# Performance work log

Measured on AMD Instinct MI355X. Metric: run time of the kernel, lower is better.

## Reference

```python
import jax, jax.numpy as jnp
import numpy as np

D_MODEL = 256
D_FFN = 1024
N_HEADS = 8
N_LEVELS = 4
N_POINTS = 4
SPATIAL = np.array([[60, 100], [30, 50], [15, 25], [8, 13]], dtype=np.int32)  # (H, W) per level


def _layer_norm(x, g, b, eps=1e-5):
    mu = jnp.mean(x, axis=-1, keepdims=True)
    var = jnp.mean(jnp.square(x - mu), axis=-1, keepdims=True)
    return (x - mu) * jax.lax.rsqrt(var + eps) * g + b


def _bilinear_sample(v_l, loc, aw, H, W):
    # v_l: (B,H,W,h,hd); loc: (B,Lq,h,p,2) normalized [0,1]; aw: (B,Lq,h,p)
    B = v_l.shape[0]
    h = v_l.shape[3]
    x = loc[..., 0] * W - 0.5  # grid_sample align_corners=False convention
    y = loc[..., 1] * H - 0.5
    x0 = jnp.floor(x)
    y0 = jnp.floor(y)
    lx = x - x0
    ly = y - y0
    x0i = x0.astype(jnp.int32)
    y0i = y0.astype(jnp.int32)
    bi = jnp.arange(B)[:, None, None, None]
    hi = jnp.arange(h)[None, None, :, None]

    def g(xi, yi):
        valid = (xi >= 0) & (xi < W) & (yi >= 0) & (yi < H)
        xc = jnp.clip(xi, 0, W - 1)
        yc = jnp.clip(yi, 0, H - 1)
        return v_l[bi, yc, xc, hi] * valid[..., None].astype(v_l.dtype)  # zero padding

    w00 = (1 - lx) * (1 - ly)
    w01 = lx * (1 - ly)
    w10 = (1 - lx) * ly
    w11 = lx * ly
    samp = (g(x0i, y0i) * w00[..., None] + g(x0i + 1, y0i) * w01[..., None]
            + g(x0i, y0i + 1) * w10[..., None] + g(x0i + 1, y0i + 1) * w11[..., None])
    # weighted sum over sampling points -> (B,Lq,h,hd)
    return jnp.einsum('blhpd,blhp->blhd', samp, aw)


def _msda(q, val, ref, W_value, b_value, W_off, b_off, W_attn, b_attn, W_out, b_out):
    # mmcv MultiScaleDeformableAttention (batch_first, identity=query, eval-mode dropout)
    B, Lq, C = q.shape
    hd = C // N_HEADS
    v = (val @ W_value + b_value).reshape(B, -1, N_HEADS, hd)
    off = (q @ W_off + b_off).reshape(B, Lq, N_HEADS, N_LEVELS, N_POINTS, 2)
    aw = jax.nn.softmax((q @ W_attn + b_attn).reshape(B, Lq, N_HEADS, N_LEVELS * N_POINTS), axis=-1)
    aw = aw.reshape(B, Lq, N_HEADS, N_LEVELS, N_POINTS)
    normalizer = jnp.asarray(SPATIAL[:, ::-1].copy(), dtype=q.dtype)  # (levels, 2) = (W, H)
    loc = ref[:, :, None, :, None, :] + off / normalizer[None, None, None, :, None, :]
    out = jnp.zeros((B, Lq, N_HEADS, hd), q.dtype)
    start = 0
    for lvl in range(N_LEVELS):
        H, W = int(SPATIAL[lvl, 0]), int(SPATIAL[lvl, 1])
        v_l = v[:, start:start + H * W].reshape(B, H, W, N_HEADS, hd)
        start += H * W
        out = out + _bilinear_sample(v_l, loc[:, :, :, lvl], aw[:, :, :, lvl], H, W)
    return q + out.reshape(B, Lq, C) @ W_out + b_out  # identity + output_proj


def setup_inputs() -> dict:
    key = jax.random.key(0)
    ks = jax.random.split(key, 16)
    bs, cams, nq = 1, 6, 6400
    l = int(SPATIAL.prod(axis=1).sum())
    s = 0.02
    inp = {
        'query': jax.random.normal(ks[0], (bs, nq, D_MODEL), jnp.float32),
        'key': jax.random.normal(ks[1], (bs, cams, l, D_MODEL), jnp.float32),
        'value': jax.random.normal(ks[2], (bs, cams, l, D_MODEL), jnp.float32),
        'reference_points_cam': jax.random.uniform(ks[3], (cams, bs, nq, N_LEVELS, 2), jnp.float32),
        'spatial_shapes': jnp.asarray(SPATIAL),
        'level_start_index': jnp.asarray(np.concatenate([[0], np.cumsum(SPATIAL.prod(axis=1))[:-1]]).astype(np.int32)),
        'bev_mask': jax.random.randint(ks[4], (cams, bs, nq, 4), 0, 2).astype(jnp.int32),
        'W_value': jax.random.normal(ks[5], (D_MODEL, D_MODEL), jnp.float32) * s,
        'b_value': jnp.zeros((D_MODEL,), jnp.float32),
        'W_off': jax.random.normal(ks[6], (D_MODEL, N_HEADS * N_LEVELS * N_POINTS * 2), jnp.float32) * s,
        'b_off': jax.random.normal(ks[7], (N_HEADS * N_LEVELS * N_POINTS * 2,), jnp.float32) * s,
        'W_attn': jax.random.normal(ks[8], (D_MODEL, N_HEADS * N_LEVELS * N_POINTS), jnp.float32) * s,
        'b_attn': jnp.zeros((N_HEADS * N_LEVELS * N_POINTS,), jnp.float32),
        'W_out': jax.random.normal(ks[9], (D_MODEL, D_MODEL), jnp.float32) * s,
        'b_out': jnp.zeros((D_MODEL,), jnp.float32),
        'ln1_g': jnp.ones((D_MODEL,), jnp.float32),
        'ln1_b': jnp.zeros((D_MODEL,), jnp.float32),
        'W1': jax.random.normal(ks[10], (D_MODEL, D_FFN), jnp.float32) * s,
        'b1': jnp.zeros((D_FFN,), jnp.float32),
        'W2': jax.random.normal(ks[11], (D_FFN, D_MODEL), jnp.float32) * s,
        'b2': jnp.zeros((D_MODEL,), jnp.float32),
        'ln2_g': jnp.ones((D_MODEL,), jnp.float32),
        'ln2_b': jnp.zeros((D_MODEL,), jnp.float32),
    }
    return inp


def reference(query, key, value, reference_points_cam, spatial_shapes, level_start_index, bev_mask,
              W_value, b_value, W_off, b_off, W_attn, b_attn, W_out, b_out,
              ln1_g, ln1_b, W1, b1, W2, b2, ln2_g, ln2_b):
    bs, nq, C = query.shape
    cams = key.shape[1]
    l = key.shape[2]
    # per-camera query visibility taken from batch element 0 (as in original)
    cam_mask = (bev_mask[:, 0].sum(-1) > 0).astype(query.dtype)  # (cams, nq)
    # rebatch via masking: equivalent to gather-to-padded since attention is per-query
    q_rb = (query[:, None] * cam_mask[None, :, :, None]).reshape(bs * cams, nq, C)
    ref_rb = (jnp.transpose(reference_points_cam, (1, 0, 2, 3, 4))
              * cam_mask[None, :, :, None, None]).reshape(bs * cams, nq, N_LEVELS, 2)
    val = value.reshape(bs * cams, l, C)
    attn = _msda(q_rb, val, ref_rb, W_value, b_value, W_off, b_off, W_attn, b_attn, W_out, b_out)
    attn = attn.reshape(bs, cams, nq, C)
    # scatter-add back (only visible camera contributions)
    slots = jnp.einsum('bknc,kn->bnc', attn, cam_mask)
    # visibility count (full bev_mask, per batch element)
    count = (bev_mask.sum(-1) > 0).astype(query.dtype)  # (cams, bs, nq)
    count = jnp.maximum(count.transpose(1, 2, 0).sum(-1), 1.0)  # (bs, nq)
    slots = slots / count[..., None]
    x = _layer_norm(slots + query, ln1_g, ln1_b)
    ffn = jax.nn.relu(x @ W1 + b1) @ W2 + b2
    return _layer_norm(x + ffn, ln2_g, ln2_b)
```

## Files before the change

### kernel.cpp

```cpp
#include <hip/hip_runtime.h>
#include <math.h>

#define NQ      6400
#define NCAMS   6
#define LTOT    7979
#define DM      256
#define DFFN    1024

typedef __attribute__((ext_vector_type(8))) short bf16x8;
typedef __attribute__((ext_vector_type(4))) float f32x4;
typedef __attribute__((ext_vector_type(2))) float f32x2;

__device__ inline unsigned short f32_to_bf16(float f) {
    unsigned u = __float_as_uint(f);
    unsigned r = u + 0x7FFF + ((u >> 16) & 1);
    return (unsigned short)(r >> 16);
}

__global__ __launch_bounds__(256) void wt_head_kernel(
    const float* __restrict__ Wv, const float* __restrict__ Woff,
    const float* __restrict__ Wattn, unsigned short* __restrict__ wsT)
{
    int b = blockIdx.x;
    const float* src; int K, N, t0, dstoff;
    if (b < 64)       { src = Wv;    K = 256; N = 256; t0 = 0;   dstoff = 0; }
    else if (b < 128) { src = Woff;  K = 256; N = 256; t0 = 64;  dstoff = 65536; }
    else              { src = Wattn; K = 256; N = 128; t0 = 128; dstoff = 131072; }
    int t = b - t0;
    int ntn = N >> 5;
    int kt = t / ntn, nt = t - kt * ntn;
    __shared__ float tile[32][33];
    int tx = threadIdx.x & 31, ty = threadIdx.x >> 5;
    #pragma unroll
    for (int i = 0; i < 4; ++i)
        tile[ty + i * 8][tx] = src[(size_t)(kt * 32 + ty + i * 8) * N + nt * 32 + tx];
    __syncthreads();
    #pragma unroll
    for (int i = 0; i < 4; ++i) {
        int nn = nt * 32 + ty + i * 8;
        wsT[dstoff + (size_t)nn * K + kt * 32 + tx] = f32_to_bf16(tile[tx][ty + i * 8]);
    }
}

__global__ __launch_bounds__(256) void head_kernel(
    const float* __restrict__ value, const float* __restrict__ query,
    const unsigned short* __restrict__ WvT, const unsigned short* __restrict__ WqT,
    const float* __restrict__ bv, const float* __restrict__ boff,
    const float* __restrict__ battn,
    unsigned char* __restrict__ vb, unsigned short* __restrict__ qoffb,
    unsigned short* __restrict__ qawb)
{
    __shared__ __align__(16) unsigned char smem[20480];
    const int b = blockIdx.x;
    const int tid = threadIdx.x;
    const int wave = tid >> 6, lane = tid & 63;
    const int wm = wave >> 1, wn = wave & 1;
    const int quad = lane >> 4, l16 = lane & 15;

    if (b < 750) {
        unsigned short (*As)[40] = (unsigned short(*)[40])smem;
        unsigned short (*Bs)[40] = (unsigned short(*)[40])(smem + 10240);
        const int m0 = (b >> 1) * 128, n0 = (b & 1) * 128;
        const int M = NCAMS * LTOT;

        f32x4 acc[4][4] = {};

        for (int k0 = 0; k0 < 256; k0 += 32) {
            #pragma unroll
            for (int i = 0; i < 2; ++i) {
                int idx = tid + 256 * i;
                int r = idx >> 2, kc = (idx & 3) * 8;
                int gr = m0 + r;
                float4 f0, f1;
                if (gr < M) {
                    f0 = *(const float4*)(value + (size_t)gr * 256 + k0 + kc);
                    f1 = *(const float4*)(value + (size_t)gr * 256 + k0 + kc + 4);
                } else { f0 = make_float4(0.f,0.f,0.f,0.f); f1 = f0; }
                uint4 o;
                o.x = f32_to_bf16(f0.x) | ((unsigned)f32_to_bf16(f0.y) << 16);
                o.y = f32_to_bf16(f0.z) | ((unsigned)f32_to_bf16(f0.w) << 16);
                o.z = f32_to_bf16(f1.x) | ((unsigned)f32_to_bf16(f1.y) << 16);
                o.w = f32_to_bf16(f1.z) | ((unsigned)f32_to_bf16(f1.w) << 16);
                *(uint4*)&As[r][kc] = o;
            }
            #pragma unroll
            for (int i = 0; i < 2; ++i) {
                int idx = tid + 256 * i;
                int r = idx >> 2, kc = (idx & 3) * 8;
                *(uint4*)&Bs[r][kc] = *(const uint4*)(WvT + (size_t)(n0 + r) * 256 + k0 + kc);
            }
            __syncthreads();
            bf16x8 af[4], bfr[4];
            #pragma unroll
            for (int mi = 0; mi < 4; ++mi)
                af[mi] = *(const bf16x8*)&As[wm * 64 + mi * 16 + l16][quad * 8];
            #pragma unroll
            for (int ni = 0; ni < 4; ++ni)
                bfr[ni] = *(const bf16x8*)&Bs[wn * 64 + ni * 16 + l16][quad * 8];
            #pragma unroll
            for (int mi = 0; mi < 4; ++mi)
                #pragma unroll
                for (int ni = 0; ni < 4; ++ni)
                    acc[mi][ni] = __builtin_amdgcn_mfma_f32_16x16x32_bf16(
                        af[mi], bfr[ni], acc[mi][ni], 0, 0, 0);
            __syncthreads();
        }

        #pragma unroll
        for (int mi = 0; mi < 4; ++mi) {
            #pragma unroll
            for (int r = 0; r < 4; ++r) {
                int gm = m0 + wm * 64 + mi * 16 + quad * 4 + r;
                if (gm >= M) continue;
                int cam = gm / LTOT;
                int pix = gm - cam * LTOT;
                #pragma unroll
                for (int ni = 0; ni < 4; ++ni) {
                    int gn = n0 + wn * 64 + ni * 16 + l16;
                    int head = gn >> 5, ch = gn & 31;
                    float v = acc[mi][ni][r] + bv[gn];
                    int p8 = __builtin_amdgcn_cvt_pk_fp8_f32(v, 0.f, 0, false);
                    vb[(((size_t)(cam * 8 + head)) * LTOT + pix) * 32 + ch] =
                        (unsigned char)(p8 & 0xFF);
                }
            }
        }
    } else {
        unsigned short (*As)[40] = (unsigned short(*)[40])smem;
        unsigned short (*Bs)[40] = (unsigned short(*)[40])(smem + 5120);
        const int t = b - 750;
        const int bx = t / 100, by = t % 100;
        const int m0 = by * 64, n0 = bx * 128;
        const int is_attn = (bx == 2);

        f32x4 acc[2][4] = {};

        for (int k0 = 0; k0 < 256; k0 += 32) {
            {
                int r = tid >> 2, kc = (tid & 3) * 8;
                float4 f0 = *(const float4*)(query + (size_t)(m0 + r) * 256 + k0 + kc);
                float4 f1 = *(const float4*)(query + (size_t)(m0 + r) * 256 + k0 + kc + 4);
                uint4 o;
                o.x = f32_to_bf16(f0.x) | ((unsigned)f32_to_bf16(f0.y) << 16);
                o.y = f32_to_bf16(f0.z) | ((unsigned)f32_to_bf16(f0.w) << 16);
                o.z = f32_to_bf16(f1.x) | ((unsigned)f32_to_bf16(f1.y) << 16);
                o.w = f32_to_bf16(f1.z) | ((unsigned)f32_to_bf16(f1.w) << 16);
                *(uint4*)&As[r][kc] = o;
            }
            #pragma unroll
            for (int i = 0; i < 2; ++i) {
                int idx = tid + 256 * i;
                int r = idx >> 2, kc = (idx & 3) * 8;
                *(uint4*)&Bs[r][kc] = *(const uint4*)(WqT + (size_t)(n0 + r) * 256 + k0 + kc);
            }
            __syncthreads();
            bf16x8 af[2], bfr[4];
            #pragma unroll
            for (int mi = 0; mi < 2; ++mi)
                af[mi] = *(const bf16x8*)&As[wm * 32 + mi * 16 + l16][quad * 8];
            #pragma unroll
            for (int ni = 0; ni < 4; ++ni)
                bfr[ni] = *(const bf16x8*)&Bs[wn * 64 + ni * 16 + l16][quad * 8];
            #pragma unroll
            for (int mi = 0; mi < 2; ++mi)
                #pragma unroll
                for (int ni = 0; ni < 4; ++ni)
                    acc[mi][ni] = __builtin_amdgcn_mfma_f32_16x16x32_bf16(
                        af[mi], bfr[ni], acc[mi][ni], 0, 0, 0);
            __syncthreads();
        }

        if (is_attn) {
            #pragma unroll
            for (int mi = 0; mi < 2; ++mi) {
                #pragma unroll
                for (int r = 0; r < 4; ++r) {
                    int gm = m0 + wm * 32 + mi * 16 + quad * 4 + r;
                    #pragma unroll
                    for (int ni = 0; ni < 4; ++ni) {
                        int gn = wn * 64 + ni * 16 + l16;
                        float v = acc[mi][ni][r] + battn[gn];
                        float mx = v;
                        #pragma unroll
                        for (int s = 1; s < 16; s <<= 1)
                            mx = fmaxf(mx, __shfl_xor(mx, s, 64));
                        float e = __expf(v - mx);
                        float sum = e;
                        #pragma unroll
                        for (int s = 1; s < 16; s <<= 1)
                            sum += __shfl_xor(sum, s, 64);
                        qawb[(size_t)gm * 128 + gn] = f32_to_bf16(e / sum);
                    }
                }
            }
        } else {
            #pragma unroll
            for (int mi = 0; mi < 2; ++mi) {
                #pragma unroll
                for (int r = 0; r < 4; ++r) {
                    int gm = m0 + wm * 32 + mi * 16 + quad * 4 + r;
                    #pragma unroll
                    for (int ni = 0; ni < 4; ++ni) {
                        int gn = n0 + wn * 64 + ni * 16 + l16;
                        qoffb[(size_t)gm * 256 + gn] = f32_to_bf16(acc[mi][ni][r] + boff[gn]);
                    }
                }
            }
        }
    }
}

__global__ __launch_bounds__(256) void sample_kernel(
    const unsigned char* __restrict__ vb,
    const unsigned short* __restrict__ qoffb,
    const unsigned short* __restrict__ qawb,
    const float* __restrict__ refpts,
    const int*   __restrict__ bev_mask,
    const float* __restrict__ Wout, const float* __restrict__ W1,
    const float* __restrict__ W2,
    unsigned short* __restrict__ outsum,
    float* __restrict__ visb,
    unsigned short* __restrict__ wsT)
{
    __shared__ unsigned s_tab[NCAMS][272][4];
    __shared__ float s_vis[NCAMS][16];
    __shared__ int   s_cnt[NCAMS];
    __shared__ int   s_nvis[16];

    const int bid = blockIdx.x;
    const int tid = threadIdx.x;

    if (bid >= 3200) {
        int t = bid - 3200;
        const float* src; int K, N, dstoff;
        if (t < 64)       { src = Wout; K = 256;  N = 256;  dstoff = 163840; }
        else if (t < 320) { src = W1;   K = 256;  N = 1024; dstoff = 229376; t -= 64; }
        else              { src = W2;   K = 1024; N = 256;  dstoff = 491520; t -= 320; }
        int ntn = N >> 5;
        int kt = t / ntn, nt = t - kt * ntn;
        float (*tile)[33] = (float(*)[33])&s_tab[0][0][0];
        int tx = tid & 31, ty = tid >> 5;
        #pragma unroll
        for (int i = 0; i < 4; ++i)
            tile[ty + i * 8][tx] = src[(size_t)(kt * 32 + ty + i * 8) * N + nt * 32 + tx];
        __syncthreads();
        #pragma unroll
        for (int i = 0; i < 4; ++i) {
            int nn = nt * 32 + ty + i * 8;
            wsT[dstoff + (size_t)nn * K + kt * 32 + tx] = f32_to_bf16(tile[tx][ty + i * 8]);
        }
        return;
    }

    const int h   = bid & 7;
    const int q0  = (bid >> 3) * 16;
    const int sq  = tid >> 4;
    const int tup = tid & 15;
    const int lvl = tup >> 2;
    const int n_s = q0 + sq;
    const int tg  = (tid >> 2) & 3;
    const int cg  = tid & 3;

    if (tid < 96) {
        int cam = tid >> 4, q = tid & 15;
        const int* bm = bev_mask + ((size_t)cam * NQ + q0 + q) * 4;
        s_vis[cam][q] = ((bm[0] + bm[1] + bm[2] + bm[3]) > 0) ? 1.f : 0.f;
    }
    __syncthreads();
    if (tid < NCAMS) {
        float s = 0.f;
        #pragma unroll
        for (int q = 0; q < 16; ++q) s += s_vis[tid][q];
        s_cnt[tid] = (int)s;
    }
    if (tid >= 32 && tid < 48) {
        int q = tid - 32;
        float s = 0.f;
        #pragma unroll
        for (int cam = 0; cam < NCAMS; ++cam) s += s_vis[cam][q];
        s_nvis[q] = (int)s;
    }

    unsigned uoff = *(const unsigned*)(qoffb + (size_t)n_s * 256 + h * 32 + tup * 2);
    const float offx  = __uint_as_float(uoff << 16);
    const float offy  = __uint_as_float(uoff & 0xFFFF0000u);
    const float my_aw = __uint_as_float((unsigned)qawb[(size_t)n_s * 128 + h * 16 + tup] << 16);
    const int Wl   = (lvl == 0) ? 100 : (lvl == 1) ? 50 : (lvl == 2) ? 25 : 13;
    const int Hl   = (lvl == 0) ? 60  : (lvl == 1) ? 30 : (lvl == 2) ? 15 : 8;
    const int base = (lvl == 0) ? 0   : (lvl == 1) ? 6000 : (lvl == 2) ? 7500 : 7875;
    const float dx = offx / (float)Wl;
    const float dy = offy / (float)Hl;
    const int tabi = sq * 17 + tup;

    float2 rp[NCAMS];
    #pragma unroll
    for (int k = 0; k < NCAMS; ++k)
        rp[k] = *(const float2*)(refpts + (((size_t)k * NQ + n_s) * 4 + lvl) * 2);
    __syncthreads();

    #pragma unroll
    for (int k = 0; k < NCAMS; ++k) {
        float fx = (rp[k].x + dx) * (float)Wl - 0.5f;
        float fy = (rp[k].y + dy) * (float)Hl - 0.5f;
        float x0f = floorf(fx), y0f = floorf(fy);
        float lx = fx - x0f, ly = fy - y0f;
        int x0 = (int)x0f, y0 = (int)y0f;
        int x1 = x0 + 1, y1 = y0 + 1;
        float wb = my_aw * s_vis[k][sq];
        float w00 = (1.f - lx) * (1.f - ly) * wb;
        float w01 = lx * (1.f - ly) * wb;
        float w10 = (1.f - lx) * ly * wb;
        float w11 = lx * ly * wb;
        bool vx0 = (x0 >= 0) & (x0 < Wl), vx1 = (x1 >= 0) & (x1 < Wl);
        bool vy0 = (y0 >= 0) & (y0 < Hl), vy1 = (y1 >= 0) & (y1 < Hl);
        uint4 o;
        o.x = (vx0 & vy0) ? (((unsigned)(base + y0 * Wl + x0) << 16) | f32_to_bf16(w00)) : 0u;
        o.y = (vx1 & vy0) ? (((unsigned)(base + y0 * Wl + x1) << 16) | f32_to_bf16(w01)) : 0u;
        o.z = (vx0 & vy1) ? (((unsigned)(base + y1 * Wl + x0) << 16) | f32_to_bf16(w10)) : 0u;
        o.w = (vx1 & vy1) ? (((unsigned)(base + y1 * Wl + x1) << 16) | f32_to_bf16(w11)) : 0u;
        *(uint4*)&s_tab[k][tabi][0] = o;
    }
    __syncthreads();

    f32x2 a01 = {0.f, 0.f}, a23 = {0.f, 0.f};
    f32x2 a45 = {0.f, 0.f}, a67 = {0.f, 0.f};

    for (int k = 0; k < NCAMS; ++k) {
        if (s_cnt[k] == 0) continue;
        const char* vkh = (const char*)vb + (size_t)(k * 8 + h) * (LTOT * 32) + cg * 8;
        #pragma unroll
        for (int j = 0; j < 4; ++j) {
            uint4 t4 = *(const uint4*)&s_tab[k][sq * 17 + tg * 4 + j][0];
            #pragma unroll
            for (int corner = 0; corner < 4; ++corner) {
                unsigned tc = (corner == 0) ? t4.x : (corner == 1) ? t4.y
                            : (corner == 2) ? t4.z : t4.w;
                float w = __uint_as_float(tc << 16);
                f32x2 w2 = {w, w};
                uint2 d = *(const uint2*)(vkh + ((size_t)(tc >> 16) << 5));
                a01 += w2 * __builtin_amdgcn_cvt_pk_f32_fp8(d.x, false);
                a23 += w2 * __builtin_amdgcn_cvt_pk_f32_fp8(d.x, true);
                a45 += w2 * __builtin_amdgcn_cvt_pk_f32_fp8(d.y, false);
                a67 += w2 * __builtin_amdgcn_cvt_pk_f32_fp8(d.y, true);
            }
        }
    }

    float a0 = a01.x, a1 = a01.y, a2 = a23.x, a3 = a23.y;
    float a4 = a45.x, a5 = a45.y, a6 = a67.x, a7 = a67.y;

    a0 += __shfl_xor(a0, 4, 64); a0 += __shfl_xor(a0, 8, 64);
    a1 += __shfl_xor(a1, 4, 64); a1 += __shfl_xor(a1, 8, 64);
    a2 += __shfl_xor(a2, 4, 64); a2 += __shfl_xor(a2, 8, 64);
    a3 += __shfl_xor(a3, 4, 64); a3 += __shfl_xor(a3, 8, 64);
    a4 += __shfl_xor(a4, 4, 64); a4 += __shfl_xor(a4, 8, 64);
    a5 += __shfl_xor(a5, 4, 64); a5 += __shfl_xor(a5, 8, 64);
    a6 += __shfl_xor(a6, 4, 64); a6 += __shfl_xor(a6, 8, 64);
    a7 += __shfl_xor(a7, 4, 64); a7 += __shfl_xor(a7, 8, 64);

    if ((tid & 12) == 0) {
        int nv = s_nvis[sq];
        float sc = 1.f / (float)(nv > 0 ? nv : 1);
        uint4 o;
        o.x = f32_to_bf16(a0 * sc) | ((unsigned)f32_to_bf16(a1 * sc) << 16);
        o.y = f32_to_bf16(a2 * sc) | ((unsigned)f32_to_bf16(a3 * sc) << 16);
        o.z = f32_to_bf16(a4 * sc) | ((unsigned)f32_to_bf16(a5 * sc) << 16);
        o.w = f32_to_bf16(a6 * sc) | ((unsigned)f32_to_bf16(a7 * sc) << 16);
        *(uint4*)(outsum + (size_t)n_s * 256 + h * 32 + cg * 8) = o;
    }
    if (h == 0 && tid < 16) visb[q0 + tid] = (s_nvis[tid] > 0) ? 1.f : 0.f;
}

__global__ __launch_bounds__(256) void projln1_ffn1_kernel(
    const unsigned short* __restrict__ A, const unsigned short* __restrict__ BT,
    const unsigned short* __restrict__ W1T,
    const float* __restrict__ query, const float* __restrict__ visb,
    const float* __restrict__ b_out, const float* __restrict__ g,
    const float* __restrict__ b, const float* __restrict__ b1,
    float* __restrict__ xout, unsigned short* __restrict__ hbf)
{
    const int K = 256;
    __shared__ __align__(16) unsigned short As[32][40];
    __shared__ __align__(16) unsigned short Bs[256][40];
    __shared__ __align__(16) unsigned short xs[32][264];
    __shared__ __align__(16) unsigned short Bs2[128][72];
    __shared__ float sred[2][4][4][2];
    __shared__ float ssred[2][4][4][2];
    __shared__ float s_mu[32], s_rs[32];

    const int tid  = threadIdx.x;
    const int wave = tid >> 6, lane = tid & 63;
    const int wm = wave >> 1, wn = wave & 1;
    const int quad = lane >> 4, l16 = lane & 15;
    const int m0 = blockIdx.x * 32;

    f32x4 acc[8] = {};

    for (int k0 = 0; k0 < K; k0 += 32) {
        {
            int r = tid >> 3, kc = (tid & 7) * 4;
            *(uint2*)&As[r][kc] = *(const uint2*)(A + (size_t)(m0 + r) * K + k0 + kc);
        }
        {
            const unsigned short* src = BT + (size_t)tid * K + k0;
            *(uint4*)&Bs[tid][0]  = *(const uint4*)(src);
            *(uint4*)&Bs[tid][8]  = *(const uint4*)(src + 8);
            *(uint4*)&Bs[tid][16] = *(const uint4*)(src + 16);
            *(uint4*)&Bs[tid][24] = *(const uint4*)(src + 24);
        }
        __syncthreads();
        bf16x8 af = *(const bf16x8*)&As[wm * 16 + l16][quad * 8];
        #pragma unroll
        for (int ni = 0; ni < 8; ++ni) {
            bf16x8 bfr = *(const bf16x8*)&Bs[wn * 128 + ni * 16 + l16][quad * 8];
            acc[ni] = __builtin_amdgcn_mfma_f32_16x16x32_bf16(af, bfr, acc[ni], 0, 0, 0);
        }
        __syncthreads();
    }

    float vals[8][4];
    #pragma unroll
    for (int r = 0; r < 4; ++r) {
        int gm = m0 + wm * 16 + quad * 4 + r;
        float vs = visb[gm];
        float s = 0.f, ss = 0.f;
        #pragma unroll
        for (int ni = 0; ni < 8; ++ni) {
            int gn = wn * 128 + ni * 16 + l16;
            float v = acc[ni][r] + vs * b_out[gn]
                    + query[(size_t)gm * 256 + gn] * (1.f + vs);
            vals[ni][r] = v;
            s += v; ss += v * v;
        }
        #pragma unroll
        for (int m = 1; m < 16; m <<= 1) {
            s  += __shfl_xor(s,  m, 64);
            ss += __shfl_xor(ss, m, 64);
        }
        if (l16 == 0) {
            sred[wm][quad][r][wn]  = s;
            ssred[wm][quad][r][wn] = ss;
        }
    }
    __syncthreads();
    if (tid < 32) {
        int lwm = tid >> 4, lq = (tid >> 2) & 3, lr = tid & 3;
        float s  = sred[lwm][lq][lr][0]  + sred[lwm][lq][lr][1];
        float ss = ssred[lwm][lq][lr][0] + ssred[lwm][lq][lr][1];
        float mu = s * (1.f / 256.f);
        float var = ss * (1.f / 256.f) - mu * mu;
        s_mu[tid] = mu;
        s_rs[tid] = rsqrtf(var + 1e-5f);
    }
    __syncthreads();

    #pragma unroll
    for (int r = 0; r < 4; ++r) {
        int rowl = wm * 16 + quad * 4 + r;
        int gm = m0 + rowl;
        float mu = s_mu[rowl], rs = s_rs[rowl];
        #pragma unroll
        for (int ni = 0; ni < 8; ++ni) {
            int gn = wn * 128 + ni * 16 + l16;
            float res = (vals[ni][r] - mu) * rs * g[gn] + b[gn];
            xout[(size_t)gm * 256 + gn] = res;
            xs[rowl][gn] = f32_to_bf16(res);
        }
    }

    for (int nc = 0; nc < 8; ++nc) {
        f32x4 acc2[4] = {};
        for (int k0 = 0; k0 < 256; k0 += 64) {
            #pragma unroll
            for (int i = 0; i < 4; ++i) {
                int idx = tid + 256 * i;
                int rr = idx >> 3, c8 = (idx & 7) * 8;
                *(uint4*)&Bs2[rr][c8] =
                    *(const uint4*)(W1T + (size_t)(nc * 128 + rr) * 256 + k0 + c8);
            }
            __syncthreads();
            #pragma unroll
            for (int s = 0; s < 2; ++s) {
                bf16x8 a2 = *(const bf16x8*)&xs[wm * 16 + l16][k0 + s * 32 + quad * 8];
                #pragma unroll
                for (int ni = 0; ni < 4; ++ni) {
                    bf16x8 b2v = *(const bf16x8*)&Bs2[wn * 64 + ni * 16 + l16][s * 32 + quad * 8];
                    acc2[ni] = __builtin_amdgcn_mfma_f32_16x16x32_bf16(a2, b2v, acc2[ni], 0, 0, 0);
                }
            }
            __syncthreads();
        }
        #pragma unroll
        for (int ni = 0; ni < 4; ++ni) {
            #pragma unroll
            for (int r = 0; r < 4; ++r) {
                int gm = m0 + wm * 16 + quad * 4 + r;
                int gn = nc * 128 + wn * 64 + ni * 16 + l16;
                float v = acc2[ni][r] + b1[gn];
                hbf[(size_t)gm * 1024 + gn] = f32_to_bf16(fmaxf(v, 0.f));
            }
        }
    }
}

__global__ __launch_bounds__(256) void gemm64_kernel(
    const unsigned short* __restrict__ A, const unsigned short* __restrict__ BT,
    const float* __restrict__ bias, unsigned short* __restrict__ Cb,
    int M, int N, int K, int mode)
{
    __shared__ __align__(16) unsigned short As[64][40];
    __shared__ __align__(16) unsigned short Bs[128][40];

    const int tid  = threadIdx.x;
    const int wave = tid >> 6, lane = tid & 63;
    const int wm = wave >> 1, wn = wave & 1;
    const int quad = lane >> 4, l16 = lane & 15;
    const int m0 = blockIdx.y * 64, n0 = blockIdx.x * 128;
    const int nz = gridDim.z;
    const int klen = K / nz;
    const int kbase = blockIdx.z * klen;

    f32x4 acc[2][4] = {};

    for (int k0 = kbase; k0 < kbase + klen; k0 += 32) {
        {
            int r = tid >> 2, kc = (tid & 3) * 8;
            int gr = m0 + r;
            uint4 d = (gr < M) ? *(const uint4*)(A + (size_t)gr * K + k0 + kc)
                               : make_uint4(0u, 0u, 0u, 0u);
            *(uint4*)&As[r][kc] = d;
        }
        #pragma unroll
        for (int i = 0; i < 2; ++i) {
            int idx = tid + 256 * i;
            int r = idx >> 2, kc = (idx & 3) * 8;
            *(uint4*)&Bs[r][kc] = *(const uint4*)(BT + (size_t)(n0 + r) * K + k0 + kc);
        }
        __syncthreads();
        bf16x8 af[2], bfr[4];
        #pragma unroll
        for (int mi = 0; mi < 2; ++mi)
            af[mi] = *(const bf16x8*)&As[wm * 32 + mi * 16 + l16][quad * 8];
        #pragma unroll
        for (int ni = 0; ni < 4; ++ni)
            bfr[ni] = *(const bf16x8*)&Bs[wn * 64 + ni * 16 + l16][quad * 8];
        #pragma unroll
        for (int mi = 0; mi < 2; ++mi)
            #pragma unroll
            for (int ni = 0; ni < 4; ++ni)
                acc[mi][ni] = __builtin_amdgcn_mfma_f32_16x16x32_bf16(
                    af[mi], bfr[ni], acc[mi][ni], 0, 0, 0);
        __syncthreads();
    }

    const float* bz = (blockIdx.z == 0) ? bias : nullptr;
    unsigned short* Cz = Cb + (size_t)blockIdx.z * M * N;

    #pragma unroll
    for (int mi = 0; mi < 2; ++mi) {
        #pragma unroll
        for (int r = 0; r < 4; ++r) {
            int gm = m0 + wm * 32 + mi * 16 + quad * 4 + r;
            if (gm >= M) continue;
            #pragma unroll
            for (int ni = 0; ni < 4; ++ni) {
                int gn = n0 + wn * 64 + ni * 16 + l16;
                float v = acc[mi][ni][r] + (bz ? bz[gn] : 0.f);
                if (mode == 1) v = fmaxf(v, 0.f);
                Cz[(size_t)gm * N + gn] = f32_to_bf16(v);
            }
        }
    }
}

__global__ __launch_bounds__(256) void ln2v_kernel(
    const float* __restrict__ x, const unsigned short* __restrict__ f0,
    const unsigned short* __restrict__ f1,
    const float* __restrict__ g, const float* __restrict__ b,
    float* __restrict__ out)
{
    int row  = blockIdx.x * 4 + (threadIdx.x >> 6);
    int lane = threadIdx.x & 63;
    size_t base = (size_t)row * 256 + lane * 4;
    float4 xv = *(const float4*)(x + base);
    uint2 u0 = *(const uint2*)(f0 + base);
    uint2 u1 = *(const uint2*)(f1 + base);
    float t0 = xv.x + __uint_as_float(u0.x << 16)        + __uint_as_float(u1.x << 16);
    float t1 = xv.y + __uint_as_float(u0.x & 0xFFFF0000u) + __uint_as_float(u1.x & 0xFFFF0000u);
    float t2 = xv.z + __uint_as_float(u0.y << 16)        + __uint_as_float(u1.y << 16);
    float t3 = xv.w + __uint_as_float(u0.y & 0xFFFF0000u) + __uint_as_float(u1.y & 0xFFFF0000u);
    float s  = t0 + t1 + t2 + t3;
    float ss = t0 * t0 + t1 * t1 + t2 * t2 + t3 * t3;
    #pragma unroll
    for (int m = 1; m < 64; m <<= 1) {
        s  += __shfl_xor(s,  m, 64);
        ss += __shfl_xor(ss, m, 64);
    }
    float mu = s * (1.f / 256.f);
    float rs = rsqrtf(ss * (1.f / 256.f) - mu * mu + 1e-5f);
    float4 gv = *(const float4*)(g + lane * 4);
    float4 bv = *(const float4*)(b + lane * 4);
    float4 o;
    o.x = (t0 - mu) * rs * gv.x + bv.x;
    o.y = (t1 - mu) * rs * gv.y + bv.y;
    o.z = (t2 - mu) * rs * gv.z + bv.z;
    o.w = (t3 - mu) * rs * gv.w + bv.w;
    *(float4*)(out + base) = o;
}

extern "C" void kernel_launch(void* const* d_in, const int* in_sizes, int n_in,
                              void* d_out, int out_size, void* d_ws, size_t ws_size,
                              hipStream_t stream)
{
    const float* query   = (const float*)d_in[0];
    const float* value   = (const float*)d_in[2];
    const float* refpts  = (const float*)d_in[3];
    const int*   bevmask = (const int*)d_in[6];
    const float* W_value = (const float*)d_in[7];
    const float* b_value = (const float*)d_in[8];
    const float* W_off   = (const float*)d_in[9];
    const float* b_off   = (const float*)d_in[10];
    const float* W_attn  = (const float*)d_in[11];
    const float* b_attn  = (const float*)d_in[12];
    const float* W_out   = (const float*)d_in[13];
    const float* b_out   = (const float*)d_in[14];
    const float* ln1_g   = (const float*)d_in[15];
    const float* ln1_b   = (const float*)d_in[16];
    const float* W1      = (const float*)d_in[17];
    const float* b1      = (const float*)d_in[18];
    const float* W2      = (const float*)d_in[19];
    const float* b2      = (const float*)d_in[20];
    const float* ln2_g   = (const float*)d_in[21];
    const float* ln2_b   = (const float*)d_in[22];
    float* out = (float*)d_out;

    char* ws = (char*)d_ws;
    unsigned char*  vb     = (unsigned char*)(ws + 0);
    float*          xbuf   = (float*)(ws + 0);
    unsigned short* hbf    = (unsigned short*)(ws + 13000000);
    unsigned short* qoffb  = (unsigned short*)(ws + 27000000);
    unsigned short* qawb   = (unsigned short*)(ws + 31000000);
    unsigned short* outsum = (unsigned short*)(ws + 33000000);
    float*          visb   = (float*)(ws + 36500000);
    unsigned short* wsT    = (unsigned short*)(ws + 36600000);
    unsigned short* ffnout = (unsigned short*)(ws + 39000000);

    unsigned short* WvT = wsT;
    unsigned short* WqT = wsT + 65536;
    unsigned short* WoT = wsT + 163840;
    unsigned short* W1T = wsT + 229376;
    unsigned short* W2T = wsT + 491520;

    wt_head_kernel<<<dim3(160), 256, 0, stream>>>(
        W_value, W_off, W_attn, wsT);
    head_kernel<<<dim3(1050), 256, 0, stream>>>(
        value, query, WvT, WqT, b_value, b_off, b_attn, vb, qoffb, qawb);
    sample_kernel<<<dim3(3776), 256, 0, stream>>>(
        vb, qoffb, qawb, refpts, bevmask, W_out, W1, W2, outsum, visb, wsT);
    projln1_ffn1_kernel<<<dim3(200), 256, 0, stream>>>(
        outsum, WoT, W1T, query, visb, b_out, ln1_g, ln1_b, b1, xbuf, hbf);
    gemm64_kernel<<<dim3(2, 100, 2), 256, 0, stream>>>(
        hbf, W2T, b2, ffnout, NQ, 256, DFFN, 2);
    ln2v_kernel<<<dim3(1600), 256, 0, stream>>>(
        xbuf, ffnout, ffnout + (size_t)NQ * 256, ln2_g, ln2_b, out);
}
```

Measured before the change: 289.7 us.

## Interleave fp8 value channels for 16-byte gathers and split FFN1 into separate GEMM

After: 283.3 us. -2.2%, faster.

```diff
diff --git a/kernel.cpp b/kernel.cpp
--- a/kernel.cpp
+++ b/kernel.cpp
@@ -115,13 +115,14 @@
                 int cam = gm / LTOT;
                 int pix = gm - cam * LTOT;
                 #pragma unroll
-                for (int ni = 0; ni < 4; ++ni) {
-                    int gn = n0 + wn * 64 + ni * 16 + l16;
-                    int head = gn >> 5, ch = gn & 31;
-                    float v = acc[mi][ni][r] + bv[gn];
-                    int p8 = __builtin_amdgcn_cvt_pk_fp8_f32(v, 0.f, 0, false);
-                    vb[(((size_t)(cam * 8 + head)) * LTOT + pix) * 32 + ch] =
-                        (unsigned char)(p8 & 0xFF);
+                for (int p = 0; p < 2; ++p) {
+                    int gn0 = n0 + wn * 64 + p * 32 + l16;
+                    int head = gn0 >> 5;
+                    float v0 = acc[mi][2 * p][r]     + bv[gn0];
+                    float v1 = acc[mi][2 * p + 1][r] + bv[gn0 + 16];
+                    int pk = __builtin_amdgcn_cvt_pk_fp8_f32(v0, v1, 0, false);
+                    *(unsigned short*)(vb + (((size_t)(cam * 8 + head)) * LTOT + pix) * 32
+                                       + 2 * l16) = (unsigned short)pk;
                 }
             }
         }
@@ -222,9 +223,8 @@
     float* __restrict__ visb,
     unsigned short* __restrict__ wsT)
 {
-    __shared__ unsigned s_tab[NCAMS][272][4];
+    __shared__ __align__(16) unsigned s_tab[NCAMS][272][4];
     __shared__ float s_vis[NCAMS][16];
-    __shared__ int   s_cnt[NCAMS];
     __shared__ int   s_nvis[16];
 
     const int bid = blockIdx.x;
@@ -244,10 +244,11 @@
         for (int i = 0; i < 4; ++i)
             tile[ty + i * 8][tx] = src[(size_t)(kt * 32 + ty + i * 8) * N + nt * 32 + tx];
         __syncthreads();
+        int txp = (dstoff == 163840) ? (((tx & 15) << 1) | (tx >> 4)) : tx;
         #pragma unroll
         for (int i = 0; i < 4; ++i) {
             int nn = nt * 32 + ty + i * 8;
-            wsT[dstoff + (size_t)nn * K + kt * 32 + tx] = f32_to_bf16(tile[tx][ty + i * 8]);
+            wsT[dstoff + (size_t)nn * K + kt * 32 + txp] = f32_to_bf16(tile[tx][ty + i * 8]);
         }
         return;
     }
@@ -258,8 +259,6 @@
     const int tup = tid & 15;
     const int lvl = tup >> 2;
     const int n_s = q0 + sq;
-    const int tg  = (tid >> 2) & 3;
-    const int cg  = tid & 3;
 
     if (tid < 96) {
         int cam = tid >> 4, q = tid & 15;
@@ -267,12 +266,6 @@
         s_vis[cam][q] = ((bm[0] + bm[1] + bm[2] + bm[3]) > 0) ? 1.f : 0.f;
     }
     __syncthreads();
-    if (tid < NCAMS) {
-        float s = 0.f;
-        #pragma unroll
-        for (int q = 0; q < 16; ++q) s += s_vis[tid][q];
-        s_cnt[tid] = (int)s;
-    }
     if (tid >= 32 && tid < 48) {
         int q = tid - 32;
         float s = 0.f;
@@ -322,68 +315,73 @@
     }
     __syncthreads();
 
-    f32x2 a01 = {0.f, 0.f}, a23 = {0.f, 0.f};
-    f32x2 a45 = {0.f, 0.f}, a67 = {0.f, 0.f};
-
+    const int tp  = (tid >> 1) & 7;
+    const int cg2 = tid & 1;
+
+    f32x2 A[8] = {};
+
+    #pragma unroll
     for (int k = 0; k < NCAMS; ++k) {
-        if (s_cnt[k] == 0) continue;
-        const char* vkh = (const char*)vb + (size_t)(k * 8 + h) * (LTOT * 32) + cg * 8;
-        #pragma unroll
-        for (int j = 0; j < 4; ++j) {
-            uint4 t4 = *(const uint4*)&s_tab[k][sq * 17 + tg * 4 + j][0];
+        const char* vkh = (const char*)vb + (size_t)(k * 8 + h) * (LTOT * 32) + cg2 * 16;
+        #pragma unroll
+        for (int t = 0; t < 2; ++t) {
+            uint4 t4 = *(const uint4*)&s_tab[k][sq * 17 + tp * 2 + t][0];
             #pragma unroll
             for (int corner = 0; corner < 4; ++corner) {
                 unsigned tc = (corner == 0) ? t4.x : (corner == 1) ? t4.y
                             : (corner == 2) ? t4.z : t4.w;
                 float w = __uint_as_float(tc << 16);
                 f32x2 w2 = {w, w};
-                uint2 d = *(const uint2*)(vkh + ((size_t)(tc >> 16) << 5));
-                a01 += w2 * __builtin_amdgcn_cvt_pk_f32_fp8(d.x, false);
-                a23 += w2 * __builtin_amdgcn_cvt_pk_f32_fp8(d.x, true);
-                a45 += w2 * __builtin_amdgcn_cvt_pk_f32_fp8(d.y, false);
-                a67 += w2 * __builtin_amdgcn_cvt_pk_f32_fp8(d.y, true);
-            }
-        }
-    }
-
-    float a0 = a01.x, a1 = a01.y, a2 = a23.x, a3 = a23.y;
-    float a4 = a45.x, a5 = a45.y, a6 = a67.x, a7 = a67.y;
-
-    a0 += __shfl_xor(a0, 4, 64); a0 += __shfl_xor(a0, 8, 64);
-    a1 += __shfl_xor(a1, 4, 64); a1 += __shfl_xor(a1, 8, 64);
-    a2 += __shfl_xor(a2, 4, 64); a2 += __shfl_xor(a2, 8, 64);
-    a3 += __shfl_xor(a3, 4, 64); a3 += __shfl_xor(a3, 8, 64);
-    a4 += __shfl_xor(a4, 4, 64); a4 += __shfl_xor(a4, 8, 64);
-    a5 += __shfl_xor(a5, 4, 64); a5 += __shfl_xor(a5, 8, 64);
-    a6 += __shfl_xor(a6, 4, 64); a6 += __shfl_xor(a6, 8, 64);
-    a7 += __shfl_xor(a7, 4, 64); a7 += __shfl_xor(a7, 8, 64);
-
-    if ((tid & 12) == 0) {
+                uint4 d = *(const uint4*)(vkh + ((size_t)(tc >> 16) << 5));
+                A[0] += w2 * __builtin_amdgcn_cvt_pk_f32_fp8(d.x, false);
+                A[1] += w2 * __builtin_amdgcn_cvt_pk_f32_fp8(d.x, true);
+                A[2] += w2 * __builtin_amdgcn_cvt_pk_f32_fp8(d.y, false);
+                A[3] += w2 * __builtin_amdgcn_cvt_pk_f32_fp8(d.y, true);
+                A[4] += w2 * __builtin_amdgcn_cvt_pk_f32_fp8(d.z, false);
+                A[5] += w2 * __builtin_amdgcn_cvt_pk_f32_fp8(d.z, true);
+                A[6] += w2 * __builtin_amdgcn_cvt_pk_f32_fp8(d.w, false);
+                A[7] += w2 * __builtin_amdgcn_cvt_pk_f32_fp8(d.w, true);
+            }
+        }
+    }
+
+    #pragma unroll
+    for (int i = 0; i < 8; ++i) {
+        float x0 = A[i].x, x1 = A[i].y;
+        x0 += __shfl_xor(x0, 2, 64); x1 += __shfl_xor(x1, 2, 64);
+        x0 += __shfl_xor(x0, 4, 64); x1 += __shfl_xor(x1, 4, 64);
+        x0 += __shfl_xor(x0, 8, 64); x1 += __shfl_xor(x1, 8, 64);
+        A[i].x = x0; A[i].y = x1;
+    }
+
+    if ((tid & 14) == 0) {
         int nv = s_nvis[sq];
         float sc = 1.f / (float)(nv > 0 ? nv : 1);
-        uint4 o;
-        o.x = f32_to_bf16(a0 * sc) | ((unsigned)f32_to_bf16(a1 * sc) << 16);
-        o.y = f32_to_bf16(a2 * sc) | ((unsigned)f32_to_bf16(a3 * sc) << 16);
-        o.z = f32_to_bf16(a4 * sc) | ((unsigned)f32_to_bf16(a5 * sc) << 16);
-        o.w = f32_to_bf16(a6 * sc) | ((unsigned)f32_to_bf16(a7 * sc) << 16);
-        *(uint4*)(outsum + (size_t)n_s * 256 + h * 32 + cg * 8) = o;
+        uint4 o0, o1;
+        o0.x = f32_to_bf16(A[0].x * sc) | ((unsigned)f32_to_bf16(A[0].y * sc) << 16);
+        o0.y = f32_to_bf16(A[1].x * sc) | ((unsigned)f32_to_bf16(A[1].y * sc) << 16);
+        o0.z = f32_to_bf16(A[2].x * sc) | ((unsigned)f32_to_bf16(A[2].y * sc) << 16);
+        o0.w = f32_to_bf16(A[3].x * sc) | ((unsigned)f32_to_bf16(A[3].y * sc) << 16);
+        o1.x = f32_to_bf16(A[4].x * sc) | ((unsigned)f32_to_bf16(A[4].y * sc) << 16);
+        o1.y = f32_to_bf16(A[5].x * sc) | ((unsigned)f32_to_bf16(A[5].y * sc) << 16);
+        o1.z = f32_to_bf16(A[6].x * sc) | ((unsigned)f32_to_bf16(A[6].y * sc) << 16);
+        o1.w = f32_to_bf16(A[7].x * sc) | ((unsigned)f32_to_bf16(A[7].y * sc) << 16);
+        *(uint4*)(outsum + (size_t)n_s * 256 + h * 32 + cg2 * 16)     = o0;
+        *(uint4*)(outsum + (size_t)n_s * 256 + h * 32 + cg2 * 16 + 8) = o1;
     }
     if (h == 0 && tid < 16) visb[q0 + tid] = (s_nvis[tid] > 0) ? 1.f : 0.f;
 }
 
-__global__ __launch_bounds__(256) void projln1_ffn1_kernel(
+__global__ __launch_bounds__(256) void projln1_kernel(
     const unsigned short* __restrict__ A, const unsigned short* __restrict__ BT,
-    const unsigned short* __restrict__ W1T,
     const float* __restrict__ query, const float* __restrict__ visb,
     const float* __restrict__ b_out, const float* __restrict__ g,
-    const float* __restrict__ b, const float* __restrict__ b1,
-    float* __restrict__ xout, unsigned short* __restrict__ hbf)
+    const float* __restrict__ b,
+    float* __restrict__ xout, unsigned short* __restrict__ xb16)
 {
     const int K = 256;
     __shared__ __align__(16) unsigned short As[32][40];
     __shared__ __align__(16) unsigned short Bs[256][40];
-    __shared__ __align__(16) unsigned short xs[32][264];
-    __shared__ __align__(16) unsigned short Bs2[128][72];
     __shared__ float sred[2][4][4][2];
     __shared__ float ssred[2][4][4][2];
     __shared__ float s_mu[32], s_rs[32];
@@ -464,41 +462,7 @@
             int gn = wn * 128 + ni * 16 + l16;
             float res = (vals[ni][r] - mu) * rs * g[gn] + b[gn];
             xout[(size_t)gm * 256 + gn] = res;
-            xs[rowl][gn] = f32_to_bf16(res);
-        }
-    }
-
-    for (int nc = 0; nc < 8; ++nc) {
-        f32x4 acc2[4] = {};
-        for (int k0 = 0; k0 < 256; k0 += 64) {
-            #pragma unroll
-            for (int i = 0; i < 4; ++i) {
-                int idx = tid + 256 * i;
-                int rr = idx >> 3, c8 = (idx & 7) * 8;
-                *(uint4*)&Bs2[rr][c8] =
-                    *(const uint4*)(W1T + (size_t)(nc * 128 + rr) * 256 + k0 + c8);
-            }
-            __syncthreads();
-            #pragma unroll
-            for (int s = 0; s < 2; ++s) {
-                bf16x8 a2 = *(const bf16x8*)&xs[wm * 16 + l16][k0 + s * 32 + quad * 8];
-                #pragma unroll
-                for (int ni = 0; ni < 4; ++ni) {
-                    bf16x8 b2v = *(const bf16x8*)&Bs2[wn * 64 + ni * 16 + l16][s * 32 + quad * 8];
-                    acc2[ni] = __builtin_amdgcn_mfma_f32_16x16x32_bf16(a2, b2v, acc2[ni], 0, 0, 0);
-                }
-            }
-            __syncthreads();
-        }
-        #pragma unroll
-        for (int ni = 0; ni < 4; ++ni) {
-            #pragma unroll
-            for (int r = 0; r < 4; ++r) {
-                int gm = m0 + wm * 16 + quad * 4 + r;
-                int gn = nc * 128 + wn * 64 + ni * 16 + l16;
-                float v = acc2[ni][r] + b1[gn];
-                hbf[(size_t)gm * 1024 + gn] = f32_to_bf16(fmaxf(v, 0.f));
-            }
+            xb16[(size_t)gm * 256 + gn] = f32_to_bf16(res);
         }
     }
 }
@@ -639,6 +603,7 @@
     float*          xbuf   = (float*)(ws + 0);
     unsigned short* hbf    = (unsigned short*)(ws + 13000000);
     unsigned short* qoffb  = (unsigned short*)(ws + 27000000);
+    unsigned short* xb16   = (unsigned short*)(ws + 27000000);
     unsigned short* qawb   = (unsigned short*)(ws + 31000000);
     unsigned short* outsum = (unsigned short*)(ws + 33000000);
     float*          visb   = (float*)(ws + 36500000);
@@ -657,8 +622,10 @@
         value, query, WvT, WqT, b_value, b_off, b_attn, vb, qoffb, qawb);
     sample_kernel<<<dim3(3776), 256, 0, stream>>>(
         vb, qoffb, qawb, refpts, bevmask, W_out, W1, W2, outsum, visb, wsT);
-    projln1_ffn1_kernel<<<dim3(200), 256, 0, stream>>>(
-        outsum, WoT, W1T, query, visb, b_out, ln1_g, ln1_b, b1, xbuf, hbf);
+    projln1_kernel<<<dim3(200), 256, 0, stream>>>(
+        outsum, WoT, query, visb, b_out, ln1_g, ln1_b, xbuf, xb16);
+    gemm64_kernel<<<dim3(8, 100, 1), 256, 0, stream>>>(
+        xb16, W1T, b1, hbf, NQ, DFFN, 256, 1);
     gemm64_kernel<<<dim3(2, 100, 2), 256, 0, stream>>>(
         hbf, W2T, b2, ffnout, NQ, 256, DFFN, 2);
     ln2v_kernel<<<dim3(1600), 256, 0, stream>>>(
```
